# Kernel optimization log

Hardware: AMD Instinct MI355X
Metric: run time of the kernel (lower is better)

## Reference

```python
import jax, jax.numpy as jnp
import numpy as np

N = 500_000   # total nodes
B = 4096      # number of graphs (segments)
D = 256       # feature dim (input_dim)
H = 4         # attention heads


def setup_inputs() -> dict:
    key = jax.random.key(0)
    ks = jax.random.split(key, 9)
    x = jax.random.normal(ks[0], (N, D), dtype=jnp.float32)
    membership = jnp.sort(jax.random.randint(ks[1], (N,), 0, B, dtype=jnp.int32))
    # xavier-normal-ish attention weight, shape (1, H, D//H)
    att_w = jax.random.normal(ks[2], (1, H, D // H), dtype=jnp.float32) * np.float32(np.sqrt(2.0 / (1 + D // H)))
    s = np.float32(1.0 / np.sqrt(D))
    gru_w_ih = jax.random.uniform(ks[3], (3 * D, D), minval=-s, maxval=s, dtype=jnp.float32)
    gru_w_hh = jax.random.uniform(ks[4], (3 * D, D), minval=-s, maxval=s, dtype=jnp.float32)
    gru_b_ih = jax.random.uniform(ks[5], (3 * D,), minval=-s, maxval=s, dtype=jnp.float32)
    gru_b_hh = jax.random.uniform(ks[6], (3 * D,), minval=-s, maxval=s, dtype=jnp.float32)
    sm = np.float32(1.0 / np.sqrt(4 * D))
    merge_w = jax.random.uniform(ks[7], (D, 4 * D), minval=-sm, maxval=sm, dtype=jnp.float32)
    merge_b = jax.random.uniform(ks[8], (D,), minval=-sm, maxval=sm, dtype=jnp.float32)
    return {"x": x, "membership": membership, "att_w": att_w,
            "gru_w_ih": gru_w_ih, "gru_w_hh": gru_w_hh,
            "gru_b_ih": gru_b_ih, "gru_b_hh": gru_b_hh,
            "merge_w": merge_w, "merge_b": merge_b}


def _readout(x, seg, att_w, gru_w_ih, gru_w_hh, gru_b_ih, gru_b_hh, merge_w, merge_b):
    n, d = x.shape
    # ---- branch 0: 'rnn-sum-max' (GRUCell on pseudo-nodes) ----
    h = jax.nn.gelu(x, approximate=False)                       # exact gelu as torch F.gelu
    center = jax.ops.segment_sum(h, seg, num_segments=B)        # op_center = 'sum'  (B, D)
    neighbor = jax.ops.segment_max(h, seg, num_segments=B)      # op_neighbor = 'max' (B, D)
    gi = center @ gru_w_ih.T + gru_b_ih                          # (B, 3D)
    gh = neighbor @ gru_w_hh.T + gru_b_hh                        # (B, 3D)
    i_r, i_z, i_n = jnp.split(gi, 3, axis=-1)
    h_r, h_z, h_n = jnp.split(gh, 3, axis=-1)
    r = jax.nn.sigmoid(i_r + h_r)
    z = jax.nn.sigmoid(i_z + h_z)
    ng = jnp.tanh(i_n + r * h_n)
    rnn_out = (1.0 - z) * ng + z * neighbor                      # (B, D)
    # ---- branch 1: 'att' (single mode, segment softmax) ----
    xv = x.reshape(n, H, d // H)
    alpha = jax.nn.leaky_relu(jnp.sum(xv * att_w, axis=-1), negative_slope=0.2)  # (N, H)
    amax = jax.ops.segment_max(alpha, seg, num_segments=B)       # (B, H)
    e = jnp.exp(alpha - amax[seg])
    denom = jax.ops.segment_sum(e, seg, num_segments=B)
    a = e / denom[seg]                                           # segment softmax (N, H)
    att_out = jax.ops.segment_sum((xv * a[:, :, None]).reshape(n, d), seg, num_segments=B)
    # ---- branch 2/3: 'max', 'sum' ----
    max_out = jax.ops.segment_max(x, seg, num_segments=B)
    sum_out = jax.ops.segment_sum(x, seg, num_segments=B)
    # ---- merge: cat + Linear ----
    merged = jnp.concatenate([rnn_out, att_out, max_out, sum_out], axis=-1)  # (B, 4D)
    return merged @ merge_w.T + merge_b                          # (B, D)


def reference(x, membership, att_w, gru_w_ih, gru_w_hh, gru_b_ih, gru_b_hh, merge_w, merge_b):
    return _readout(x, membership, att_w, gru_w_ih, gru_w_hh, gru_b_ih, gru_b_hh, merge_w, merge_b)
```

## Files before the change

kernel.cpp:

```cpp
#include <hip/hip_runtime.h>
#include <math.h>
#include <stdint.h>

#define NN 500000
#define NB 4096
#define DD 256

typedef short  short8  __attribute__((ext_vector_type(8)));
typedef short  short4v __attribute__((ext_vector_type(4)));
typedef float  floatx4 __attribute__((ext_vector_type(4)));
typedef float  f2      __attribute__((ext_vector_type(2)));

__device__ __forceinline__ f2 sp(float v) { return (f2){v, v}; }

__device__ __forceinline__ short f2bf(float f) {
    uint32_t u = __float_as_uint(f);
    u += 0x7fffu + ((u >> 16) & 1u);
    return (short)(u >> 16);
}

__device__ __forceinline__ f2 gelu2(f2 x) {
    f2 z = __builtin_elementwise_abs(x) * sp(0.70710678118654752440f);
    f2 p = __builtin_elementwise_fma(z, sp(0.0000430638f), sp(0.0002765672f));
    p = __builtin_elementwise_fma(p, z, sp(0.0001520143f));
    p = __builtin_elementwise_fma(p, z, sp(0.0092705272f));
    p = __builtin_elementwise_fma(p, z, sp(0.0422820123f));
    p = __builtin_elementwise_fma(p, z, sp(0.0705230784f));
    p = __builtin_elementwise_fma(p, z, sp(1.0f));
    p = p * p; p = p * p; p = p * p; p = p * p;
    f2 r = { __builtin_amdgcn_rcpf(p.x), __builtin_amdgcn_rcpf(p.y) };
    f2 er = __builtin_elementwise_copysign(sp(1.0f) - r, x);
    return sp(0.5f) * x * (sp(1.0f) + er);
}

__global__ __launch_bounds__(256) void seg_bounds(
    const int* __restrict__ seg, int* __restrict__ bnd)
{
    int i = blockIdx.x * 256 + threadIdx.x;
    if (i >= NN) return;
    int s = seg[i];
    if (i == 0) {
        for (int b = 0; b <= s; ++b) bnd[b] = 0;
    } else {
        int p = seg[i - 1];
        for (int b = p + 1; b <= s; ++b) bnd[b] = i;
    }
    if (i == NN - 1) {
        for (int b = s + 1; b <= NB; ++b) bnd[b] = NN;
    }
}

__global__ __launch_bounds__(256, 8) void seg_kernel(
    const float* __restrict__ x,
    const int*   __restrict__ bnd,
    const float* __restrict__ att_w,
    float* __restrict__ merged,
    float* __restrict__ center,
    float* __restrict__ neighbor)
{
    const int b   = blockIdx.x;
    const int tid = threadIdx.x;
    const int w   = tid >> 6;
    const int l   = tid & 63;

    const int start = bnd[b];
    const int end   = bnd[b + 1];

    const int cnt = end - start;
    const int q = cnt >> 2, r = cnt & 3;
    const int my_start = start + w * q + (w < r ? w : r);
    const int my_cnt   = q + (w < r ? 1 : 0);

    const float4 awv = *reinterpret_cast<const float4*>(&att_w[4 * l]);
    const f2 aw01 = {awv.x, awv.y}, aw23 = {awv.z, awv.w};

    f2 c01 = sp(0.f), c23 = sp(0.f);
    f2 s01 = sp(0.f), s23 = sp(0.f);
    f2 m01 = sp(-INFINITY), m23 = sp(-INFINITY);
    f2 a01 = sp(0.f), a23 = sp(0.f);
    float lsum = 0.f;

    auto process = [&](const float4& v) {
        f2 vl = {v.x, v.y}, vh = {v.z, v.w};
        f2 gl = gelu2(vl), gh = gelu2(vh);
        c01 += gl; c23 += gh;
        s01 += vl; s23 += vh;
        m01 = __builtin_elementwise_max(m01, vl);
        m23 = __builtin_elementwise_max(m23, vh);
        f2 tp = __builtin_elementwise_fma(vh, aw23, vl * aw01);
        float t = tp.x + tp.y;
        t += __shfl_xor(t, 1, 64);
        t += __shfl_xor(t, 2, 64);
        t += __shfl_xor(t, 4, 64);
        t += __shfl_xor(t, 8, 64);
        float alpha = fmaxf(t, 0.2f * t);
        float e = __expf(alpha);
        lsum += e;
        f2 ev = sp(e);
        a01 = __builtin_elementwise_fma(ev, vl, a01);
        a23 = __builtin_elementwise_fma(ev, vh, a23);
    };

    const float* __restrict__ xl = x + 4 * l;
    auto LD = [&](int row) -> float4 {
        int rc = row < (NN - 1) ? row : (NN - 1);
        return *reinterpret_cast<const float4*>(&xl[(size_t)rc * DD]);
    };

    float4 q0 = LD(my_start),     q1 = LD(my_start + 1),
           q2 = LD(my_start + 2), q3 = LD(my_start + 3);
    int ip = my_start + 4;
    int rem = my_cnt;
    while (rem >= 2) {
        float4 f0 = LD(ip), f1 = LD(ip + 1);
        process(q0); process(q1);
        q0 = q2; q1 = q3; q2 = f0; q3 = f1;
        ip += 2; rem -= 2;
    }
    if (rem) process(q0);

    __shared__ float lds[4][4][256];
    __shared__ float ldsl[4][4];
    const int c = 4 * l;
    lds[0][w][c+0] = c01.x; lds[0][w][c+1] = c01.y; lds[0][w][c+2] = c23.x; lds[0][w][c+3] = c23.y;
    lds[1][w][c+0] = s01.x; lds[1][w][c+1] = s01.y; lds[1][w][c+2] = s23.x; lds[1][w][c+3] = s23.y;
    lds[2][w][c+0] = m01.x; lds[2][w][c+1] = m01.y; lds[2][w][c+2] = m23.x; lds[2][w][c+3] = m23.y;
    lds[3][w][c+0] = a01.x; lds[3][w][c+1] = a01.y; lds[3][w][c+2] = a23.x; lds[3][w][c+3] = a23.y;
    if ((l & 15) == 0) ldsl[w][l >> 4] = lsum;
    __syncthreads();

    const int d = tid;
    float cs = lds[0][0][d] + lds[0][1][d] + lds[0][2][d] + lds[0][3][d];
    float ss = lds[1][0][d] + lds[1][1][d] + lds[1][2][d] + lds[1][3][d];
    float mm = fmaxf(fmaxf(lds[2][0][d], lds[2][1][d]), fmaxf(lds[2][2][d], lds[2][3][d]));
    float ac = lds[3][0][d] + lds[3][1][d] + lds[3][2][d] + lds[3][3][d];
    const int h = d >> 6;
    float denom = ldsl[0][h] + ldsl[1][h] + ldsl[2][h] + ldsl[3][h];
    float att = (denom > 0.f) ? ac / denom : 0.f;
    float nm = gelu2((f2){mm, mm}).x;

    float* mrow = merged + (size_t)b * 1024;
    mrow[256 + d] = att;
    mrow[512 + d] = mm;
    mrow[768 + d] = ss;
    center  [(size_t)b * DD + d] = cs;
    neighbor[(size_t)b * DD + d] = nm;
}

__global__ __launch_bounds__(256) void gemm_gru(
    const float* __restrict__ center,
    const float* __restrict__ neighbor,
    const float* __restrict__ w_ih,
    const float* __restrict__ w_hh,
    const float* __restrict__ b_ih,
    const float* __restrict__ b_hh,
    float* __restrict__ merged)
{
    __shared__ short Ac[64 * 40];
    __shared__ short An[64 * 40];
    __shared__ short Wt[6][16 * 40];

    const int t   = threadIdx.x;
    const int w   = t >> 6, l = t & 63;
    const int m0  = blockIdx.x * 64;
    const int j0  = blockIdx.y * 16;
    const int lr  = t >> 2;
    const int lc  = (t & 3) * 8;
    const int l15 = l & 15, lq = l >> 4;

    int wg[3], wrow[3], wk4[3];
    const float* wbase[3];
    #pragma unroll
    for (int i = 0; i < 3; ++i) {
        int f = i * 256 + t;
        wg[i] = f >> 7;
        int rem2 = f & 127;
        wrow[i] = rem2 >> 3;
        wk4[i]  = rem2 & 7;
        wbase[i] = (wg[i] < 3)
            ? &w_ih[(size_t)(wg[i] * 256 + j0 + wrow[i]) * 256 + wk4[i] * 4]
            : &w_hh[(size_t)((wg[i] - 3) * 256 + j0 + wrow[i]) * 256 + wk4[i] * 4];
    }
    const float* crp = &center  [(size_t)(m0 + lr) * 256 + lc];
    const float* nrp = &neighbor[(size_t)(m0 + lr) * 256 + lc];

    floatx4 acc[6] = {};

    float4 c0 = *(const float4*)(crp),     c1 = *(const float4*)(crp + 4);
    float4 e0 = *(const float4*)(nrp),     e1 = *(const float4*)(nrp + 4);
    float4 v0 = *(const float4*)(wbase[0]);
    float4 v1 = *(const float4*)(wbase[1]);
    float4 v2 = *(const float4*)(wbase[2]);

    for (int k0 = 0; k0 < 256; k0 += 32) {
        const int kn = (k0 + 32 < 256) ? k0 + 32 : k0;
        float4 nc0 = *(const float4*)(crp + kn), nc1 = *(const float4*)(crp + kn + 4);
        float4 ne0 = *(const float4*)(nrp + kn), ne1 = *(const float4*)(nrp + kn + 4);
        float4 nv0 = *(const float4*)(wbase[0] + kn);
        float4 nv1 = *(const float4*)(wbase[1] + kn);
        float4 nv2 = *(const float4*)(wbase[2] + kn);

        short8 a8 = { f2bf(c0.x), f2bf(c0.y), f2bf(c0.z), f2bf(c0.w),
                      f2bf(c1.x), f2bf(c1.y), f2bf(c1.z), f2bf(c1.w) };
        short8 n8 = { f2bf(e0.x), f2bf(e0.y), f2bf(e0.z), f2bf(e0.w),
                      f2bf(e1.x), f2bf(e1.y), f2bf(e1.z), f2bf(e1.w) };
        short4v w40 = { f2bf(v0.x), f2bf(v0.y), f2bf(v0.z), f2bf(v0.w) };
        short4v w41 = { f2bf(v1.x), f2bf(v1.y), f2bf(v1.z), f2bf(v1.w) };
        short4v w42 = { f2bf(v2.x), f2bf(v2.y), f2bf(v2.z), f2bf(v2.w) };

        __syncthreads();
        *(short8*)&Ac[lr * 40 + lc] = a8;
        *(short8*)&An[lr * 40 + lc] = n8;
        *(short4v*)&Wt[wg[0]][wrow[0] * 40 + wk4[0] * 4] = w40;
        *(short4v*)&Wt[wg[1]][wrow[1] * 40 + wk4[1] * 4] = w41;
        *(short4v*)&Wt[wg[2]][wrow[2] * 40 + wk4[2] * 4] = w42;
        __syncthreads();

        short8 afc = *(short8*)&Ac[(w * 16 + l15) * 40 + lq * 8];
        short8 afn = *(short8*)&An[(w * 16 + l15) * 40 + lq * 8];
        #pragma unroll
        for (int gg = 0; gg < 6; ++gg) {
            short8 bf = *(short8*)&Wt[gg][l15 * 40 + lq * 8];
            acc[gg] = __builtin_amdgcn_mfma_f32_16x16x32_bf16(
                (gg < 3) ? afc : afn, bf, acc[gg], 0, 0, 0);
        }

        c0 = nc0; c1 = nc1; e0 = ne0; e1 = ne1;
        v0 = nv0; v1 = nv1; v2 = nv2;
    }

    const int col = j0 + l15;
    const float bir = b_ih[col], biz = b_ih[256 + col], bin = b_ih[512 + col];
    const float bhr = b_hh[col], bhz = b_hh[256 + col], bhn = b_hh[512 + col];
    #pragma unroll
    for (int qq = 0; qq < 4; ++qq) {
        const int row = m0 + w * 16 + lq * 4 + qq;
        float rr = 1.f / (1.f + __expf(-(acc[0][qq] + bir + acc[3][qq] + bhr)));
        float zz = 1.f / (1.f + __expf(-(acc[1][qq] + biz + acc[4][qq] + bhz)));
        float ng = tanhf(acc[2][qq] + bin + rr * (acc[5][qq] + bhn));
        float nb = neighbor[(size_t)row * 256 + col];
        merged[(size_t)row * 1024 + col] = (1.f - zz) * ng + zz * nb;
    }
}

__global__ __launch_bounds__(256) void gemm_bf16(
    const float* __restrict__ A, const float* __restrict__ W,
    const float* __restrict__ bias, float* __restrict__ C, int K, int ldc)
{
    __shared__ short As[32 * 72];
    __shared__ short Bs[64 * 72];

    const int t   = threadIdx.x;
    const int w   = t >> 6, l = t & 63;
    const int wm  = w >> 1, wn = w & 1;
    const int m0  = blockIdx.x * 32, n0 = blockIdx.y * 64;
    const int arow = t >> 3, ak = (t & 7) * 8;
    const int brow = t >> 2, bk = (t & 3) * 16;
    const int l15 = l & 15, lq = l >> 4;

    const float* ap = &A[(size_t)(m0 + arow) * K + ak];
    const float* bp = &W[(size_t)(n0 + brow) * K + bk];

    floatx4 acc[2] = {};

    float4 a0 = *(const float4*)(ap),      a1 = *(const float4*)(ap + 4);
    float4 b0 = *(const float4*)(bp),      b1 = *(const float4*)(bp + 4);
    float4 b2 = *(const float4*)(bp + 8),  b3 = *(const float4*)(bp + 12);

    for (int k0 = 0; k0 < K; k0 += 64) {
        const int kn = (k0 + 64 < K) ? k0 + 64 : k0;
        float4 na0 = *(const float4*)(ap + kn),      na1 = *(const float4*)(ap + kn + 4);
        float4 nb0 = *(const float4*)(bp + kn),      nb1 = *(const float4*)(bp + kn + 4);
        float4 nb2 = *(const float4*)(bp + kn + 8),  nb3 = *(const float4*)(bp + kn + 12);

        short8 a8  = { f2bf(a0.x), f2bf(a0.y), f2bf(a0.z), f2bf(a0.w),
                       f2bf(a1.x), f2bf(a1.y), f2bf(a1.z), f2bf(a1.w) };
        short8 w80 = { f2bf(b0.x), f2bf(b0.y), f2bf(b0.z), f2bf(b0.w),
                       f2bf(b1.x), f2bf(b1.y), f2bf(b1.z), f2bf(b1.w) };
        short8 w81 = { f2bf(b2.x), f2bf(b2.y), f2bf(b2.z), f2bf(b2.w),
                       f2bf(b3.x), f2bf(b3.y), f2bf(b3.z), f2bf(b3.w) };

        __syncthreads();
        *(short8*)&As[arow * 72 + ak]     = a8;
        *(short8*)&Bs[brow * 72 + bk]     = w80;
        *(short8*)&Bs[brow * 72 + bk + 8] = w81;
        __syncthreads();

        #pragma unroll
        for (int ks = 0; ks < 2; ++ks) {
            short8 af  = *(short8*)&As[(wm * 16 + l15) * 72 + ks * 32 + lq * 8];
            short8 bf0 = *(short8*)&Bs[(wn * 32 +      l15) * 72 + ks * 32 + lq * 8];
            short8 bf1 = *(short8*)&Bs[(wn * 32 + 16 + l15) * 72 + ks * 32 + lq * 8];
            acc[0] = __builtin_amdgcn_mfma_f32_16x16x32_bf16(af, bf0, acc[0], 0, 0, 0);
            acc[1] = __builtin_amdgcn_mfma_f32_16x16x32_bf16(af, bf1, acc[1], 0, 0, 0);
        }

        a0 = na0; a1 = na1; b0 = nb0; b1 = nb1; b2 = nb2; b3 = nb3;
    }

    #pragma unroll
    for (int jj = 0; jj < 2; ++jj) {
        const int col = n0 + wn * 32 + 16 * jj + l15;
        const float bv = bias[col];
        #pragma unroll
        for (int qq = 0; qq < 4; ++qq) {
            const int row = m0 + wm * 16 + lq * 4 + qq;
            C[(size_t)row * ldc + col] = acc[jj][qq] + bv;
        }
    }
}

extern "C" void kernel_launch(void* const* d_in, const int* in_sizes, int n_in,
                              void* d_out, int out_size, void* d_ws, size_t ws_size,
                              hipStream_t stream) {
    const float* x       = (const float*)d_in[0];
    const int*   seg     = (const int*)  d_in[1];
    const float* att_w   = (const float*)d_in[2];
    const float* w_ih    = (const float*)d_in[3];
    const float* w_hh    = (const float*)d_in[4];
    const float* b_ih    = (const float*)d_in[5];
    const float* b_hh    = (const float*)d_in[6];
    const float* merge_w = (const float*)d_in[7];
    const float* merge_b = (const float*)d_in[8];
    float* out = (float*)d_out;

    float* ws       = (float*)d_ws;
    float* merged   = ws;
    float* center   = merged   + (size_t)NB * 1024;
    float* neighbor = center   + (size_t)NB * DD;
    int*   bnd      = (int*)(neighbor + (size_t)NB * DD);

    seg_bounds<<<(NN + 255) / 256, 256, 0, stream>>>(seg, bnd);

    seg_kernel<<<NB, 256, 0, stream>>>(x, bnd, att_w, merged, center, neighbor);

    dim3 gg(NB / 64, DD / 16);
    gemm_gru<<<gg, 256, 0, stream>>>(center, neighbor, w_ih, w_hh, b_ih, b_hh, merged);

    dim3 g2(NB / 32, DD / 64);
    gemm_bf16<<<g2, 256, 0, stream>>>(merged, merge_w, merge_b, out, 1024, DD);
}
```

Before: 150.8 us.

## Stream node rows through LDS ring via global_load_lds with 8-deep prefetch

Replaces the register double-buffered row loads in the segment reduction kernel with asynchronous global-to-LDS loads into a per-wave 8-slot ring buffer, with explicit vmcnt waits to keep up to 8 rows in flight. The goal is more memory-level parallelism over the streamed x rows without holding prefetched data in registers. It drops the occupancy hint from launch bounds and adds 32 KB of LDS per block, which may lower occupancy. The hand-written waitcnt and sched barriers also constrain compiler scheduling.

```diff
diff --git a/kernel.cpp b/kernel.cpp
--- a/kernel.cpp
+++ b/kernel.cpp
@@ -10,6 +10,9 @@
 typedef short  short4v __attribute__((ext_vector_type(4)));
 typedef float  floatx4 __attribute__((ext_vector_type(4)));
 typedef float  f2      __attribute__((ext_vector_type(2)));
+
+typedef const __attribute__((address_space(1))) unsigned int g_u32;
+typedef       __attribute__((address_space(3))) unsigned int l_u32;
 
 __device__ __forceinline__ f2 sp(float v) { return (f2){v, v}; }
 
@@ -33,6 +36,20 @@
     return sp(0.5f) * x * (sp(1.0f) + er);
 }
 
+__device__ __forceinline__ void wait_vmcnt(int n) {
+    switch (n) {
+    case 0: asm volatile("s_waitcnt vmcnt(0)" ::: "memory"); break;
+    case 1: asm volatile("s_waitcnt vmcnt(1)" ::: "memory"); break;
+    case 2: asm volatile("s_waitcnt vmcnt(2)" ::: "memory"); break;
+    case 3: asm volatile("s_waitcnt vmcnt(3)" ::: "memory"); break;
+    case 4: asm volatile("s_waitcnt vmcnt(4)" ::: "memory"); break;
+    case 5: asm volatile("s_waitcnt vmcnt(5)" ::: "memory"); break;
+    case 6: asm volatile("s_waitcnt vmcnt(6)" ::: "memory"); break;
+    default: asm volatile("s_waitcnt vmcnt(7)" ::: "memory"); break;
+    }
+    __builtin_amdgcn_sched_barrier(0);
+}
+
 __global__ __launch_bounds__(256) void seg_bounds(
     const int* __restrict__ seg, int* __restrict__ bnd)
 {
@@ -50,7 +67,7 @@
     }
 }
 
-__global__ __launch_bounds__(256, 8) void seg_kernel(
+__global__ __launch_bounds__(256) void seg_kernel(
     const float* __restrict__ x,
     const int*   __restrict__ bnd,
     const float* __restrict__ att_w,
@@ -58,6 +75,10 @@
     float* __restrict__ center,
     float* __restrict__ neighbor)
 {
+    __shared__ __align__(16) float ring[4][8][256];
+    __shared__ float lds[4][4][256];
+    __shared__ float ldsl[4][4];
+
     const int b   = blockIdx.x;
     const int tid = threadIdx.x;
     const int w   = tid >> 6;
@@ -73,6 +94,8 @@
 
     const float4 awv = *reinterpret_cast<const float4*>(&att_w[4 * l]);
     const f2 aw01 = {awv.x, awv.y}, aw23 = {awv.z, awv.w};
+    asm volatile("" :: "v"(awv.x), "v"(awv.y), "v"(awv.z), "v"(awv.w));
+    asm volatile("s_waitcnt vmcnt(0)" ::: "memory");
 
     f2 c01 = sp(0.f), c23 = sp(0.f);
     f2 s01 = sp(0.f), s23 = sp(0.f);
@@ -101,26 +124,28 @@
         a23 = __builtin_elementwise_fma(ev, vh, a23);
     };
 
-    const float* __restrict__ xl = x + 4 * l;
-    auto LD = [&](int row) -> float4 {
+    auto ISSUE = [&](int row, int slot) {
         int rc = row < (NN - 1) ? row : (NN - 1);
-        return *reinterpret_cast<const float4*>(&xl[(size_t)rc * DD]);
+        __builtin_amdgcn_global_load_lds(
+            (g_u32*)(x + (size_t)rc * DD + 4 * l),
+            (l_u32*)(&ring[w][slot][0]), 16, 0, 0);
     };
 
-    float4 q0 = LD(my_start),     q1 = LD(my_start + 1),
-           q2 = LD(my_start + 2), q3 = LD(my_start + 3);
-    int ip = my_start + 4;
-    int rem = my_cnt;
-    while (rem >= 2) {
-        float4 f0 = LD(ip), f1 = LD(ip + 1);
-        process(q0); process(q1);
-        q0 = q2; q1 = q3; q2 = f0; q3 = f1;
-        ip += 2; rem -= 2;
-    }
-    if (rem) process(q0);
-
-    __shared__ float lds[4][4][256];
-    __shared__ float ldsl[4][4];
+    const int P = my_cnt < 8 ? my_cnt : 8;
+    for (int i = 0; i < P; ++i) ISSUE(my_start + i, i);
+
+    for (int i = 0; i < my_cnt; ++i) {
+        int n = my_cnt - i - 1;
+        wait_vmcnt(n < 7 ? n : 7);
+        const int slot = i & 7;
+        float4 v = *reinterpret_cast<const float4*>(&ring[w][slot][4 * l]);
+        process(v);
+        asm volatile("s_waitcnt lgkmcnt(0)" ::: "memory");
+        __builtin_amdgcn_sched_barrier(0);
+        const int nx = i + 8;
+        if (nx < my_cnt) ISSUE(my_start + nx, slot);
+    }
+
     const int c = 4 * l;
     lds[0][w][c+0] = c01.x; lds[0][w][c+1] = c01.y; lds[0][w][c+2] = c23.x; lds[0][w][c+3] = c23.y;
     lds[1][w][c+0] = s01.x; lds[1][w][c+1] = s01.y; lds[1][w][c+2] = s23.x; lds[1][w][c+3] = s23.y;
```

After: 193.3 us. 28.2% more time.

## Split segment reduction across two column halves per segment

Applied to the files above, without the earlier changes.

The segment reduction kernel now launches two blocks per graph, each covering 128 of the 256 feature columns. Each lane loads a float2 instead of a float4, and the attention dot-product shuffle reduction grows to 32 lanes so each head's 64 columns are still reduced correctly. This doubles the number of blocks to raise parallelism and memory-level concurrency, at the cost of narrower loads, duplicated boundary and index work, and a dropped occupancy hint in launch_bounds.

```diff
diff --git a/kernel.cpp b/kernel.cpp
--- a/kernel.cpp
+++ b/kernel.cpp
@@ -50,7 +50,7 @@
     }
 }
 
-__global__ __launch_bounds__(256, 8) void seg_kernel(
+__global__ __launch_bounds__(256) void seg_kernel(
     const float* __restrict__ x,
     const int*   __restrict__ bnd,
     const float* __restrict__ att_w,
@@ -59,6 +59,8 @@
     float* __restrict__ neighbor)
 {
     const int b   = blockIdx.x;
+    const int h2  = blockIdx.y;
+    const int c0  = h2 * 128;
     const int tid = threadIdx.x;
     const int w   = tid >> 6;
     const int l   = tid & 63;
@@ -71,80 +73,80 @@
     const int my_start = start + w * q + (w < r ? w : r);
     const int my_cnt   = q + (w < r ? 1 : 0);
 
-    const float4 awv = *reinterpret_cast<const float4*>(&att_w[4 * l]);
-    const f2 aw01 = {awv.x, awv.y}, aw23 = {awv.z, awv.w};
-
-    f2 c01 = sp(0.f), c23 = sp(0.f);
-    f2 s01 = sp(0.f), s23 = sp(0.f);
-    f2 m01 = sp(-INFINITY), m23 = sp(-INFINITY);
-    f2 a01 = sp(0.f), a23 = sp(0.f);
+    const f2 aw = *reinterpret_cast<const f2*>(&att_w[c0 + 2 * l]);
+
+    f2 cS = sp(0.f);
+    f2 sS = sp(0.f);
+    f2 mS = sp(-INFINITY);
+    f2 aS = sp(0.f);
     float lsum = 0.f;
 
-    auto process = [&](const float4& v) {
-        f2 vl = {v.x, v.y}, vh = {v.z, v.w};
-        f2 gl = gelu2(vl), gh = gelu2(vh);
-        c01 += gl; c23 += gh;
-        s01 += vl; s23 += vh;
-        m01 = __builtin_elementwise_max(m01, vl);
-        m23 = __builtin_elementwise_max(m23, vh);
-        f2 tp = __builtin_elementwise_fma(vh, aw23, vl * aw01);
+    auto process = [&](const f2& v) {
+        f2 g = gelu2(v);
+        cS += g;
+        sS += v;
+        mS = __builtin_elementwise_max(mS, v);
+        f2 tp = v * aw;
         float t = tp.x + tp.y;
         t += __shfl_xor(t, 1, 64);
         t += __shfl_xor(t, 2, 64);
         t += __shfl_xor(t, 4, 64);
         t += __shfl_xor(t, 8, 64);
+        t += __shfl_xor(t, 16, 64);
         float alpha = fmaxf(t, 0.2f * t);
         float e = __expf(alpha);
         lsum += e;
-        f2 ev = sp(e);
-        a01 = __builtin_elementwise_fma(ev, vl, a01);
-        a23 = __builtin_elementwise_fma(ev, vh, a23);
+        aS = __builtin_elementwise_fma(sp(e), v, aS);
     };
 
-    const float* __restrict__ xl = x + 4 * l;
-    auto LD = [&](int row) -> float4 {
+    const float* __restrict__ xl = x + c0 + 2 * l;
+    auto LD = [&](int row) -> f2 {
         int rc = row < (NN - 1) ? row : (NN - 1);
-        return *reinterpret_cast<const float4*>(&xl[(size_t)rc * DD]);
+        return *reinterpret_cast<const f2*>(&xl[(size_t)rc * DD]);
     };
 
-    float4 q0 = LD(my_start),     q1 = LD(my_start + 1),
-           q2 = LD(my_start + 2), q3 = LD(my_start + 3);
+    f2 q0 = LD(my_start),     q1 = LD(my_start + 1),
+       q2 = LD(my_start + 2), q3 = LD(my_start + 3);
     int ip = my_start + 4;
     int rem = my_cnt;
     while (rem >= 2) {
-        float4 f0 = LD(ip), f1 = LD(ip + 1);
+        f2 f0 = LD(ip), f1 = LD(ip + 1);
         process(q0); process(q1);
         q0 = q2; q1 = q3; q2 = f0; q3 = f1;
         ip += 2; rem -= 2;
     }
     if (rem) process(q0);
 
-    __shared__ float lds[4][4][256];
-    __shared__ float ldsl[4][4];
-    const int c = 4 * l;
-    lds[0][w][c+0] = c01.x; lds[0][w][c+1] = c01.y; lds[0][w][c+2] = c23.x; lds[0][w][c+3] = c23.y;
-    lds[1][w][c+0] = s01.x; lds[1][w][c+1] = s01.y; lds[1][w][c+2] = s23.x; lds[1][w][c+3] = s23.y;
-    lds[2][w][c+0] = m01.x; lds[2][w][c+1] = m01.y; lds[2][w][c+2] = m23.x; lds[2][w][c+3] = m23.y;
-    lds[3][w][c+0] = a01.x; lds[3][w][c+1] = a01.y; lds[3][w][c+2] = a23.x; lds[3][w][c+3] = a23.y;
-    if ((l & 15) == 0) ldsl[w][l >> 4] = lsum;
+    __shared__ float lds[4][4][128];
+    __shared__ float ldsl[4][2];
+    const int c = 2 * l;
+    lds[0][w][c] = cS.x; lds[0][w][c+1] = cS.y;
+    lds[1][w][c] = sS.x; lds[1][w][c+1] = sS.y;
+    lds[2][w][c] = mS.x; lds[2][w][c+1] = mS.y;
+    lds[3][w][c] = aS.x; lds[3][w][c+1] = aS.y;
+    if ((l & 31) == 0) ldsl[w][l >> 5] = lsum;
     __syncthreads();
 
-    const int d = tid;
-    float cs = lds[0][0][d] + lds[0][1][d] + lds[0][2][d] + lds[0][3][d];
-    float ss = lds[1][0][d] + lds[1][1][d] + lds[1][2][d] + lds[1][3][d];
-    float mm = fmaxf(fmaxf(lds[2][0][d], lds[2][1][d]), fmaxf(lds[2][2][d], lds[2][3][d]));
-    float ac = lds[3][0][d] + lds[3][1][d] + lds[3][2][d] + lds[3][3][d];
-    const int h = d >> 6;
-    float denom = ldsl[0][h] + ldsl[1][h] + ldsl[2][h] + ldsl[3][h];
-    float att = (denom > 0.f) ? ac / denom : 0.f;
-    float nm = gelu2((f2){mm, mm}).x;
-
-    float* mrow = merged + (size_t)b * 1024;
-    mrow[256 + d] = att;
-    mrow[512 + d] = mm;
-    mrow[768 + d] = ss;
-    center  [(size_t)b * DD + d] = cs;
-    neighbor[(size_t)b * DD + d] = nm;
+    if (tid < 128) {
+        const int d = tid;
+        float cs = lds[0][0][d] + lds[0][1][d] + lds[0][2][d] + lds[0][3][d];
+        float ss = lds[1][0][d] + lds[1][1][d] + lds[1][2][d] + lds[1][3][d];
+        float mm = fmaxf(fmaxf(lds[2][0][d], lds[2][1][d]),
+                         fmaxf(lds[2][2][d], lds[2][3][d]));
+        float ac = lds[3][0][d] + lds[3][1][d] + lds[3][2][d] + lds[3][3][d];
+        const int hl = d >> 6;
+        float denom = ldsl[0][hl] + ldsl[1][hl] + ldsl[2][hl] + ldsl[3][hl];
+        float att = (denom > 0.f) ? ac / denom : 0.f;
+        float nm = gelu2((f2){mm, mm}).x;
+
+        const int gcol = c0 + d;
+        float* mrow = merged + (size_t)b * 1024;
+        mrow[256 + gcol] = att;
+        mrow[512 + gcol] = mm;
+        mrow[768 + gcol] = ss;
+        center  [(size_t)b * DD + gcol] = cs;
+        neighbor[(size_t)b * DD + gcol] = nm;
+    }
 }
 
 __global__ __launch_bounds__(256) void gemm_gru(
@@ -332,7 +334,8 @@
 
     seg_bounds<<<(NN + 255) / 256, 256, 0, stream>>>(seg, bnd);
 
-    seg_kernel<<<NB, 256, 0, stream>>>(x, bnd, att_w, merged, center, neighbor);
+    dim3 gs(NB, 2);
+    seg_kernel<<<gs, 256, 0, stream>>>(x, bnd, att_w, merged, center, neighbor);
 
     dim3 gg(NB / 64, DD / 16);
     gemm_gru<<<gg, 256, 0, stream>>>(center, neighbor, w_ih, w_hh, b_ih, b_hh, merged);
```

Result: slower. 159.8 us (+6.0%).
